# Optimization experiments

Hardware: AMD Instinct MI355X
Metric: run time of the kernel (lower is better)

The kernel has to match this reference:

```python
import jax, jax.numpy as jnp
import numpy as np

N = 16777216  # batch*A*width*height (flat anchor-score vector)
BINS = 10
LOSS_WEIGHT = 1.0


def setup_inputs() -> dict:
    key = jax.random.key(0)
    k1, k2, k3 = jax.random.split(key, 3)
    pred = jax.random.normal(k1, (N,), dtype=jnp.float32)          # IoU logits
    target = jax.random.uniform(k2, (N,), dtype=jnp.float32)       # IoU targets in [0,1]
    label_weight = (jax.random.uniform(k3, (N,)) > 0.3).astype(jnp.float32)  # 1=valid, 0=ignore
    return {"pred": pred, "target": target, "label_weight": label_weight, "bins": BINS}


def reference(pred, target, label_weight, bins):
    # target is detached in the original module
    target = jax.lax.stop_gradient(target)
    # gradient norm g = |sigmoid(pred).detach() - target|, lies in [0,1]
    g = jnp.abs(jax.lax.stop_gradient(jax.nn.sigmoid(pred)) - target)
    valid = label_weight > 0
    validf = valid.astype(jnp.float32)
    tot = jnp.maximum(jnp.sum(validf), 1.0)

    # edges are i/bins with last edge nudged by 1e-6, so bin = floor(g*bins) clipped to bins-1
    bin_idx = jnp.clip((g * bins).astype(jnp.int32), 0, bins - 1)
    counts = jax.ops.segment_sum(validf, bin_idx, num_segments=bins)  # per-bin valid counts
    n = jnp.sum(counts > 0).astype(jnp.float32)                        # number of nonempty bins
    counts_safe = jnp.maximum(counts, 1.0)
    w_per_bin = jnp.where(counts > 0, tot / counts_safe, 0.0) / jnp.maximum(n, 1.0)
    weights = jnp.where(valid, w_per_bin[bin_idx], 0.0)

    # weighted BCE-with-logits, reduction='sum', stable form: logaddexp(0,x) - x*z
    bce = jnp.logaddexp(0.0, pred) - pred * target
    loss = jnp.sum(weights * bce) / tot
    return loss * LOSS_WEIGHT
```

## Files before the change

kernel.cpp:

```cpp
#include <hip/hip_runtime.h>

#define BINS 10
#define REPLICAS 16
#define NBLOCKS 2048
#define NTHREADS 256


__global__ __launch_bounds__(NTHREADS, 4)
void ghm_pass1(const float* __restrict__ pred,
               const float* __restrict__ target,
               const float* __restrict__ lw,
               float* __restrict__ rep_sums,
               unsigned int* __restrict__ rep_cnts,
               int n)
{
    __shared__ float ls[BINS];
    __shared__ unsigned int lc[BINS];
    if (threadIdx.x < BINS) { ls[threadIdx.x] = 0.0f; lc[threadIdx.x] = 0u; }

    float s0=0.f,s1=0.f,s2=0.f,s3=0.f,s4=0.f,s5=0.f,s6=0.f,s7=0.f,s8=0.f,s9=0.f;
    unsigned long long cpk = 0ull;

#define SBIN(B, S) { (S) += (bi_ == (B)) ? bce_ : 0.0f; }
#define PROC(P, T, W) do {                                                     \
    float p_ = (P), t_ = (T);                                                  \
    float ap_ = fabsf(p_);                                                     \
    float q_  = __builtin_amdgcn_exp2f(ap_ * -1.4426950408889634f); \
    float r_  = __builtin_amdgcn_rcpf(1.0f + q_);                              \
    float sig_ = (p_ >= 0.0f) ? r_ : (1.0f - r_);                              \
    float g_   = fabsf(sig_ - t_);                                             \
    int bi_ = (int)(g_ * 10.0f);                                               \
    bi_ = bi_ > 9 ? 9 : bi_;                                                   \
    bi_ = ((W) > 0.0f) ? bi_ : 10;              \
    float bce_ = fmaxf(p_, 0.0f)                                               \
               + 0.6931471805599453f * __builtin_amdgcn_logf(1.0f + q_)        \
               - p_ * t_;                                                      \
    cpk += 1ull << (6 * bi_);                                                  \
    SBIN(0,s0) SBIN(1,s1) SBIN(2,s2) SBIN(3,s3) SBIN(4,s4)                     \
    SBIN(5,s5) SBIN(6,s6) SBIN(7,s7) SBIN(8,s8) SBIN(9,s9)                     \
} while (0)
#define PROC4(PV, TV, WV) {                                                    \
    PROC((PV).x, (TV).x, (WV).x);                                              \
    PROC((PV).y, (TV).y, (WV).y);                                              \
    PROC((PV).z, (TV).z, (WV).z);                                              \
    PROC((PV).w, (TV).w, (WV).w); }

    const int gid = blockIdx.x * NTHREADS + threadIdx.x;
    const int stride = NBLOCKS * NTHREADS;
    const int n4 = n >> 2;
    const float4* p4 = (const float4*)pred;
    const float4* t4 = (const float4*)target;
    const float4* w4 = (const float4*)lw;
    for (int i = gid; i < n4; i += stride) {
        float4 pv = p4[i];
        float4 tv = t4[i];
        float4 wv = w4[i];
        PROC4(pv, tv, wv);
    }
    for (int j = (n4 << 2) + gid; j < n; j += stride) {
        PROC(pred[j], target[j], lw[j]);
    }

    unsigned int c0 = (unsigned int)(cpk       ) & 63u;
    unsigned int c1 = (unsigned int)(cpk >>  6 ) & 63u;
    unsigned int c2 = (unsigned int)(cpk >> 12 ) & 63u;
    unsigned int c3 = (unsigned int)(cpk >> 18 ) & 63u;
    unsigned int c4 = (unsigned int)(cpk >> 24 ) & 63u;
    unsigned int c5 = (unsigned int)(cpk >> 30 ) & 63u;
    unsigned int c6 = (unsigned int)(cpk >> 36 ) & 63u;
    unsigned int c7 = (unsigned int)(cpk >> 42 ) & 63u;
    unsigned int c8 = (unsigned int)(cpk >> 48 ) & 63u;
    unsigned int c9 = (unsigned int)(cpk >> 54 ) & 63u;

#define WREDUCE(S, C) {                                                        \
    _Pragma("unroll")                                                          \
    for (int o_ = 32; o_ > 0; o_ >>= 1) {                                      \
        (S) += __shfl_down((S), o_, 64);                                       \
        (C) += __shfl_down((C), o_, 64);                                       \
    } }
    WREDUCE(s0,c0) WREDUCE(s1,c1) WREDUCE(s2,c2) WREDUCE(s3,c3) WREDUCE(s4,c4)
    WREDUCE(s5,c5) WREDUCE(s6,c6) WREDUCE(s7,c7) WREDUCE(s8,c8) WREDUCE(s9,c9)

    __syncthreads();
    if ((threadIdx.x & 63) == 0) {
        atomicAdd(&ls[0], s0); atomicAdd(&lc[0], c0);
        atomicAdd(&ls[1], s1); atomicAdd(&lc[1], c1);
        atomicAdd(&ls[2], s2); atomicAdd(&lc[2], c2);
        atomicAdd(&ls[3], s3); atomicAdd(&lc[3], c3);
        atomicAdd(&ls[4], s4); atomicAdd(&lc[4], c4);
        atomicAdd(&ls[5], s5); atomicAdd(&lc[5], c5);
        atomicAdd(&ls[6], s6); atomicAdd(&lc[6], c6);
        atomicAdd(&ls[7], s7); atomicAdd(&lc[7], c7);
        atomicAdd(&ls[8], s8); atomicAdd(&lc[8], c8);
        atomicAdd(&ls[9], s9); atomicAdd(&lc[9], c9);
    }
    __syncthreads();
    if (threadIdx.x < BINS) {
        int rep = blockIdx.x & (REPLICAS - 1);
        atomicAdd(&rep_sums[rep * BINS + threadIdx.x], ls[threadIdx.x]);
        atomicAdd(&rep_cnts[rep * BINS + threadIdx.x], lc[threadIdx.x]);
    }
#undef PROC
#undef PROC4
#undef SBIN
#undef WREDUCE
}

__global__ void ghm_finalize(const float* __restrict__ rep_sums,
                             const unsigned int* __restrict__ rep_cnts,
                             float* __restrict__ out)
{
    __shared__ double S[BINS];
    __shared__ unsigned int C[BINS];
    int t = threadIdx.x;
    if (t < BINS) {
        double s = 0.0;
        unsigned int cc = 0u;
        for (int r = 0; r < REPLICAS; ++r) {
            s += (double)rep_sums[r * BINS + t];
            cc += rep_cnts[r * BINS + t];
        }
        S[t] = s;
        C[t] = cc;
    }
    __syncthreads();
    if (t == 0) {
        double n_ne = 0.0;
        for (int b = 0; b < BINS; ++b) if (C[b] > 0u) n_ne += 1.0;
        double nn = n_ne > 1.0 ? n_ne : 1.0;
        double loss = 0.0;
        for (int b = 0; b < BINS; ++b)
            if (C[b] > 0u) loss += S[b] / ((double)C[b] * nn);
        out[0] = (float)loss;
    }
}

extern "C" void kernel_launch(void* const* d_in, const int* in_sizes, int n_in,
                              void* d_out, int out_size, void* d_ws, size_t ws_size,
                              hipStream_t stream)
{
    const float* pred = (const float*)d_in[0];
    const float* target = (const float*)d_in[1];
    const float* lw = (const float*)d_in[2];
    int n = in_sizes[0];

    float* rep_sums = (float*)d_ws;
    unsigned int* rep_cnts =
        (unsigned int*)((char*)d_ws + REPLICAS * BINS * sizeof(float));

    hipMemsetAsync(d_ws, 0, 2 * REPLICAS * BINS * sizeof(float), stream);
    ghm_pass1<<<NBLOCKS, NTHREADS, 0, stream>>>(pred, target, lw,
                                                rep_sums, rep_cnts, n);
    ghm_finalize<<<1, 64, 0, stream>>>(rep_sums, rep_cnts, (float*)d_out);
}
```

Before: 203.9 us.

## Software-pipeline blocked loads with double prefetch and nontemporal hints

Each block now processes a contiguous chunk of float4 groups. A two-deep register prefetch keeps loads for future iterations in flight while the current one is computed, and sched_barrier stops the compiler from reordering them. Loads use nontemporal hints because the streamed data is not reused. This aims to hide memory latency in a loop with only a few loads in flight per thread, at the cost of higher register pressure.

```diff
diff --git a/kernel.cpp b/kernel.cpp
--- a/kernel.cpp
+++ b/kernel.cpp
@@ -5,6 +5,8 @@
 #define NBLOCKS 2048
 #define NTHREADS 256
 
+
+typedef float vfloat4 __attribute__((ext_vector_type(4)));
 
 __global__ __launch_bounds__(NTHREADS, 4)
 void ghm_pass1(const float* __restrict__ pred,
@@ -45,16 +47,38 @@
     PROC((PV).z, (TV).z, (WV).z);                                              \
     PROC((PV).w, (TV).w, (WV).w); }
 
+    const int n4 = n >> 2;
+    const int full = n4 / (NBLOCKS * NTHREADS);
+    const vfloat4* p4 = (const vfloat4*)pred;
+    const vfloat4* t4 = (const vfloat4*)target;
+    const vfloat4* w4 = (const vfloat4*)lw;
+
+    if (full >= 2) {
+        const int base = blockIdx.x * full * NTHREADS + threadIdx.x;
+        vfloat4 pA = __builtin_nontemporal_load(&p4[base]);
+        vfloat4 tA = __builtin_nontemporal_load(&t4[base]);
+        vfloat4 wA = __builtin_nontemporal_load(&w4[base]);
+        vfloat4 pB = __builtin_nontemporal_load(&p4[base + NTHREADS]);
+        vfloat4 tB = __builtin_nontemporal_load(&t4[base + NTHREADS]);
+        vfloat4 wB = __builtin_nontemporal_load(&w4[base + NTHREADS]);
+        __builtin_amdgcn_sched_barrier(0);
+        for (int j = 2; j < full; ++j) {
+            const int idx = base + j * NTHREADS;
+            vfloat4 pC = __builtin_nontemporal_load(&p4[idx]);
+            vfloat4 tC = __builtin_nontemporal_load(&t4[idx]);
+            vfloat4 wC = __builtin_nontemporal_load(&w4[idx]);
+            __builtin_amdgcn_sched_barrier(0);
+            PROC4(pA, tA, wA);
+            pA = pB; tA = tB; wA = wB;
+            pB = pC; tB = tC; wB = wC;
+        }
+        PROC4(pA, tA, wA);
+        PROC4(pB, tB, wB);
+    }
     const int gid = blockIdx.x * NTHREADS + threadIdx.x;
     const int stride = NBLOCKS * NTHREADS;
-    const int n4 = n >> 2;
-    const float4* p4 = (const float4*)pred;
-    const float4* t4 = (const float4*)target;
-    const float4* w4 = (const float4*)lw;
-    for (int i = gid; i < n4; i += stride) {
-        float4 pv = p4[i];
-        float4 tv = t4[i];
-        float4 wv = w4[i];
+    for (int i = full * stride + gid; i < n4; i += stride) {
+        vfloat4 pv = p4[i], tv = t4[i], wv = w4[i];
         PROC4(pv, tv, wv);
     }
     for (int j = (n4 << 2) + gid; j < n; j += stride) {
@@ -148,7 +172,7 @@
     unsigned int* rep_cnts =
         (unsigned int*)((char*)d_ws + REPLICAS * BINS * sizeof(float));
 
-    hipMemsetAsync(d_ws, 0, 2 * REPLICAS * BINS * sizeof(float), stream);
+    (void)hipMemsetAsync(d_ws, 0, 2 * REPLICAS * BINS * sizeof(float), stream);
     ghm_pass1<<<NBLOCKS, NTHREADS, 0, stream>>>(pred, target, lw,
                                                 rep_sums, rep_cnts, n);
     ghm_finalize<<<1, 64, 0, stream>>>(rep_sums, rep_cnts, (float*)d_out);
```

Result: faster. 184.6 us (-9.5%).
